# Optimization experiments

Measured on AMD Instinct MI355X. Metric: run time of the kernel, lower is better.

## Reference

```python
import jax, jax.numpy as jnp
import numpy as np

N_NODES = 100000
N_EDGES = 1600000
IN_DIM = 75
H_COMP = 64
H_BOND = 16
DEPTH = 3


def setup_inputs() -> dict:
    key = jax.random.key(0)
    ks = jax.random.split(key, 8)
    x = jax.random.normal(ks[0], (N_NODES, IN_DIM), dtype=jnp.float32)
    edge_index = jax.random.randint(ks[1], (2, N_EDGES), 0, N_NODES, dtype=jnp.int64)
    edge_attr = jax.random.normal(ks[2], (N_EDGES, H_BOND), dtype=jnp.float32)
    proj_w = jax.random.normal(ks[3], (IN_DIM, H_COMP), dtype=jnp.float32) * (1.0 / np.sqrt(IN_DIM))
    proj_b = jnp.zeros((H_COMP,), dtype=jnp.float32)
    u2_w = jax.random.normal(ks[4], (DEPTH, H_COMP + H_BOND, H_COMP), dtype=jnp.float32) * (1.0 / np.sqrt(H_COMP + H_BOND))
    u2_b = jnp.zeros((DEPTH, H_COMP), dtype=jnp.float32)
    u1_w = jax.random.normal(ks[5], (DEPTH, 2 * H_COMP, H_COMP), dtype=jnp.float32) * (1.0 / np.sqrt(2 * H_COMP))
    u1_b = jnp.zeros((DEPTH, H_COMP), dtype=jnp.float32)
    return {"x": x, "edge_index": edge_index, "edge_attr": edge_attr,
            "proj_w": proj_w, "proj_b": proj_b,
            "u2_w": u2_w, "u2_b": u2_b, "u1_w": u1_w, "u1_b": u1_b}


def reference(x, edge_index, edge_attr, proj_w, proj_b, u2_w, u2_b, u1_w, u1_b):
    # PyG default flow source_to_target: messages gathered from edge_index[0],
    # scatter-added at edge_index[1].
    src, dst = edge_index[0], edge_index[1]
    n = x.shape[0]
    # input projection: [N, in_dim] -> [N, H]
    h = x @ proj_w + proj_b
    for l in range(u2_w.shape[0]):
        # message: concat(x_j, edge_attr) -> Linear -> LeakyReLU(0.1)   [E, H+B] -> [E, H]
        z = jnp.concatenate([h[src], edge_attr], axis=-1)
        m = jax.nn.leaky_relu(z @ u2_w[l] + u2_b[l], negative_slope=0.1)
        # aggregate: scatter-add over destination nodes  [E, H] -> [N, H]
        agg = jax.ops.segment_sum(m, dst, num_segments=n)
        # update: concat(x, agg) -> Linear  [N, 2H] -> [N, H]
        h = jnp.concatenate([h, agg], axis=-1) @ u1_w[l] + u1_b[l]
    return h
```

## Files before the change

kernel.cpp:

```cpp
#include <hip/hip_runtime.h>

typedef __attribute__((ext_vector_type(8))) short frag_ab;
typedef __attribute__((ext_vector_type(4))) float frag_cd;

__device__ __forceinline__ short f2bf(float f) {
  union { float f; unsigned u; } v; v.f = f;
  unsigned r = v.u + 0x7fffu + ((v.u >> 16) & 1u);
  return (short)(r >> 16);
}
__device__ __forceinline__ float bf2f(short s) {
  union { unsigned u; float f; } v; v.u = ((unsigned)(unsigned short)s) << 16;
  return v.f;
}

__device__ __forceinline__ void wconv_body(
    const float* __restrict__ W, short* __restrict__ out,
    int Keff, int S, int nmat, int tid)
{
  int per = S * 4 * 64;
  if (tid >= nmat * per) return;
  int m = tid / per, r = tid % per;
  int s = r / 256, ct = (r >> 6) & 3, ln = r & 63;
  const float* Wm = W + (size_t)m * Keff * 64;
  __align__(16) short tmp[8];
  for (int j = 0; j < 8; ++j) {
    int k = s * 32 + (ln >> 4) * 8 + j;
    int n = ct * 16 + (ln & 15);
    tmp[j] = (k < Keff) ? f2bf(Wm[k * 64 + n]) : (short)0;
  }
  *(uint4*)&out[((size_t)m * per + (size_t)(s * 4 + ct) * 64 + ln) * 8] = *(uint4*)tmp;
}

__global__ void wconv_all(const float* __restrict__ pw,
                          const float* __restrict__ u2w,
                          const float* __restrict__ u1w,
                          short* projt, short* u2t, short* u1t)
{
  int b = blockIdx.x, t = threadIdx.x;
  if (b < 3)        wconv_body(pw,  projt, 75,  3, 1, b * 256 + t);
  else if (b < 12)  wconv_body(u2w, u2t,   80,  3, 3, (b - 3) * 256 + t);
  else              wconv_body(u1w, u1t,   128, 4, 3, (b - 12) * 256 + t);
}

#define AS1 104
__global__ __launch_bounds__(256, 4) void proj_kernel(
    const float* __restrict__ x, const short* __restrict__ wt,
    const float* __restrict__ bias, short* __restrict__ hbf, int N)
{
  __shared__ __align__(16) short A[128 * AS1];
  int t = threadIdx.x;
  int nb = blockIdx.x * 128;
  int ln = t & 63;
  frag_ab bf[12];
  for (int s = 0; s < 3; ++s)
    for (int ct = 0; ct < 4; ++ct)
      bf[s * 4 + ct] = *(const frag_ab*)&wt[((size_t)(s * 4 + ct) * 64 + ln) * 8];
  for (int i = 0; i < 48; ++i) {
    int q = i * 256 + t; int el = q / 96; int c = q - el * 96;
    int rg = nb + el;
    float v = (c < 75 && rg < N) ? x[rg * 75 + c] : 0.f;
    A[el * AS1 + c] = f2bf(v);
  }
  __syncthreads();
  int wv = t >> 6;
  int lrow = ln & 15, lk = ln >> 4;
  frag_cd acc[2][4];
  for (int rt = 0; rt < 2; ++rt) for (int ct = 0; ct < 4; ++ct) {
    frag_cd z = {0.f, 0.f, 0.f, 0.f}; acc[rt][ct] = z;
  }
  for (int s = 0; s < 3; ++s) {
    frag_ab a0 = *(const frag_ab*)&A[(wv*32 + lrow) * AS1 + s*32 + lk*8];
    frag_ab a1 = *(const frag_ab*)&A[(wv*32 + 16 + lrow) * AS1 + s*32 + lk*8];
    for (int ct = 0; ct < 4; ++ct) {
      acc[0][ct] = __builtin_amdgcn_mfma_f32_16x16x32_bf16(a0, bf[s*4+ct], acc[0][ct], 0, 0, 0);
      acc[1][ct] = __builtin_amdgcn_mfma_f32_16x16x32_bf16(a1, bf[s*4+ct], acc[1][ct], 0, 0, 0);
    }
  }
  float bv[4];
  for (int ct = 0; ct < 4; ++ct) bv[ct] = bias[ct*16 + lrow];
  for (int rt = 0; rt < 2; ++rt)
    for (int ct = 0; ct < 4; ++ct)
      for (int r = 0; r < 4; ++r) {
        int row = wv*32 + rt*16 + lk*4 + r;
        int rg = nb + row;
        if (rg < N) hbf[(size_t)rg * 64 + ct*16 + lrow] = f2bf(acc[rt][ct][r] + bv[ct]);
      }
}

__global__ __launch_bounds__(256) void hist_kernel(
    const int* __restrict__ dst, int* __restrict__ counts,
    int* __restrict__ rank, int E)
{
  int i = blockIdx.x * 256 + threadIdx.x;
  if (i < E) rank[i] = atomicAdd(&counts[dst[i]], 1);
}

#define SCAN_TILE 2048
__global__ __launch_bounds__(256) void scan_k1(
    const int* __restrict__ counts, int* __restrict__ offsets,
    int* __restrict__ bsum, int n)
{
  __shared__ int ts[256];
  int t = threadIdx.x;
  int base = blockIdx.x * SCAN_TILE + t * 8;
  int v[8]; int s = 0;
  for (int j = 0; j < 8; ++j) { v[j] = (base + j < n) ? counts[base + j] : 0; s += v[j]; }
  ts[t] = s; __syncthreads();
  for (int off = 1; off < 256; off <<= 1) {
    int x = (t >= off) ? ts[t - off] : 0;
    __syncthreads();
    ts[t] += x;
    __syncthreads();
  }
  if (t == 255) bsum[blockIdx.x] = ts[255];
  int run = (t > 0) ? ts[t - 1] : 0;
  for (int j = 0; j < 8; ++j) { if (base + j < n) offsets[base + j] = run; run += v[j]; }
}

__global__ __launch_bounds__(256) void scan_k3(
    int* __restrict__ offsets, const int* __restrict__ bsum, int n, int nb)
{
  __shared__ int adds;
  int t = threadIdx.x;
  if (t < 64) {
    int v = (t < nb) ? bsum[t] : 0;
    int x = v;
    for (int o = 1; o < 64; o <<= 1) { int y = __shfl_up(x, o); if (t >= o) x += y; }
    int b = blockIdx.x;
    int a = __shfl(x, b - 1);
    if (t == 0) adds = (b == 0) ? 0 : a;
  }
  __syncthreads();
  int add = adds;
  int base = blockIdx.x * SCAN_TILE + t;
  for (int j = 0; j < 8; ++j) { int i = base + j * 256; if (i < n) offsets[i] += add; }
}

__global__ __launch_bounds__(256) void scatter_kernel(
    const int* __restrict__ src, const int* __restrict__ dst,
    const float* __restrict__ attr, const int* __restrict__ offsets,
    const int* __restrict__ rank, uint4* __restrict__ rec, int E)
{
  int e = blockIdx.x * 256 + threadIdx.x;
  if (e < E) {
    int d = dst[e];
    int p = offsets[d] + rank[e];
    const float4* a4 = (const float4*)(attr + (size_t)e * 16);
    float4 v0 = a4[0], v1 = a4[1], v2 = a4[2], v3 = a4[3];
    __align__(16) short tmp[16];
    tmp[0]=f2bf(v0.x); tmp[1]=f2bf(v0.y); tmp[2]=f2bf(v0.z); tmp[3]=f2bf(v0.w);
    tmp[4]=f2bf(v1.x); tmp[5]=f2bf(v1.y); tmp[6]=f2bf(v1.z); tmp[7]=f2bf(v1.w);
    tmp[8]=f2bf(v2.x); tmp[9]=f2bf(v2.y); tmp[10]=f2bf(v2.z); tmp[11]=f2bf(v2.w);
    tmp[12]=f2bf(v3.x); tmp[13]=f2bf(v3.y); tmp[14]=f2bf(v3.z); tmp[15]=f2bf(v3.w);
    uint4* rp = rec + (size_t)p * 4;
    uint4 q0; q0.x = (unsigned)src[e]; q0.y = (unsigned)d; q0.z = 0u; q0.w = 0u;
    uint4 qz = {0u, 0u, 0u, 0u};
    rp[0] = q0;
    rp[1] = *(uint4*)&tmp[0];
    rp[2] = *(uint4*)&tmp[8];
    rp[3] = qz;
  }
}

#define MS 66
__global__ __launch_bounds__(256, 6) void msg_kernel(
    const short* __restrict__ hbf, const uint4* __restrict__ rec,
    const short* __restrict__ wt, const float* __restrict__ bias,
    float* __restrict__ agg, int E)
{
  __shared__ short M2[128 * MS];
  int t = threadIdx.x;
  int eb = blockIdx.x * 128;
  int ln = t & 63;
  int wv = t >> 6;
  int lrow = ln & 15, lk = ln >> 4;
  int lo = wv * 32;

  int g0 = eb + lo + lrow;
  int g1 = g0 + 16;
  int p0 = g0 > E - 1 ? E - 1 : g0;
  int p1 = g1 > E - 1 ? E - 1 : g1;
  int2 sd0 = *(const int2*)(rec + (size_t)p0 * 4);
  int2 sd1 = *(const int2*)(rec + (size_t)p1 * 4);
  int d0 = (g0 < E) ? sd0.y : -1;
  int d1 = (g1 < E) ? sd1.y : -1;

  frag_ab a[3][2];
  a[0][0] = *(const frag_ab*)&hbf[(size_t)sd0.x * 64 + lk*8];
  a[0][1] = *(const frag_ab*)&hbf[(size_t)sd1.x * 64 + lk*8];
  a[1][0] = *(const frag_ab*)&hbf[(size_t)sd0.x * 64 + 32 + lk*8];
  a[1][1] = *(const frag_ab*)&hbf[(size_t)sd1.x * 64 + 32 + lk*8];
  frag_ab z8 = {0,0,0,0,0,0,0,0};
  a[2][0] = (lk < 2) ? *(const frag_ab*)((const short*)(rec + (size_t)p0 * 4) + 8 + lk*8) : z8;
  a[2][1] = (lk < 2) ? *(const frag_ab*)((const short*)(rec + (size_t)p1 * 4) + 8 + lk*8) : z8;

  frag_cd acc[2][4];
  for (int rt = 0; rt < 2; ++rt) for (int ct = 0; ct < 4; ++ct) {
    frag_cd z = {0.f, 0.f, 0.f, 0.f}; acc[rt][ct] = z;
  }
  for (int s = 0; s < 3; ++s)
    for (int ct = 0; ct < 4; ++ct) {
      frag_ab b = *(const frag_ab*)&wt[((size_t)(s * 4 + ct) * 64 + ln) * 8];
      acc[0][ct] = __builtin_amdgcn_mfma_f32_16x16x32_bf16(a[s][0], b, acc[0][ct], 0, 0, 0);
      acc[1][ct] = __builtin_amdgcn_mfma_f32_16x16x32_bf16(a[s][1], b, acc[1][ct], 0, 0, 0);
    }
  float bv[4];
  for (int ct = 0; ct < 4; ++ct) bv[ct] = bias[ct*16 + lrow];

  for (int rt = 0; rt < 2; ++rt)
    for (int ct = 0; ct < 4; ++ct)
      for (int r = 0; r < 4; ++r) {
        int row = lo + rt*16 + lk*4 + r;
        float m = acc[rt][ct][r] + bv[ct];
        m = m > 0.f ? m : 0.1f * m;
        M2[row * MS + ct*16 + lrow] = f2bf(m);
      }
  __asm__ __volatile__("s_waitcnt lgkmcnt(0)" ::: "memory");

  int dl = (ln < 16) ? d0 : d1;
  int dnext = __shfl_down(dl, 1);
  bool end = (ln < 32) && ((ln == 31) || (dl != dnext));
  unsigned em = (unsigned)__ballot(end);
  unsigned cm = em & ~(em & (0u - em)) & 0x7fffffffu;

  float s = 0.f;
#pragma unroll
  for (int i = 0; i < 32; ++i) {
    s += bf2f(M2[(lo + i) * MS + ln]);
    if ((em >> i) & 1u) {
      int di = (i < 16) ? __shfl(d0, i) : __shfl(d1, i - 16);
      if (di >= 0) {
        float* dest = &agg[(size_t)di * 64 + ln];
        if ((cm >> i) & 1u) *dest = s;
        else unsafeAtomicAdd(dest, s);
      }
      s = 0.f;
    }
  }
}

__global__ __launch_bounds__(256, 4) void upd_kernel(
    const short* __restrict__ hbf, float* __restrict__ agg,
    const short* __restrict__ wt, const float* __restrict__ bias,
    float* __restrict__ hout, short* __restrict__ hbfo, int N, int last)
{
  int t = threadIdx.x;
  int nb = blockIdx.x * 64;
  int ln = t & 63;
  int wv = t >> 6;
  int lrow = ln & 15, lk = ln >> 4;
  int r0 = nb + wv*16 + lrow;

  frag_ab z8 = {0,0,0,0,0,0,0,0};
  frag_ab a[4];
  a[0] = (r0 < N) ? *(const frag_ab*)&hbf[(size_t)r0 * 64 + lk*8]      : z8;
  a[1] = (r0 < N) ? *(const frag_ab*)&hbf[(size_t)r0 * 64 + 32 + lk*8] : z8;
  for (int si = 0; si < 2; ++si) {
    int cb = si * 32 + lk * 8;
    frag_ab af = z8;
    if (r0 < N) {
      float* ap = &agg[(size_t)r0 * 64 + cb];
      float4 v0 = *(const float4*)ap;
      float4 v1 = *(const float4*)(ap + 4);
      af[0]=f2bf(v0.x); af[1]=f2bf(v0.y); af[2]=f2bf(v0.z); af[3]=f2bf(v0.w);
      af[4]=f2bf(v1.x); af[5]=f2bf(v1.y); af[6]=f2bf(v1.z); af[7]=f2bf(v1.w);
      if (!last) {
        float4 z = make_float4(0.f, 0.f, 0.f, 0.f);
        *(float4*)ap = z; *(float4*)(ap + 4) = z;
      }
    }
    a[2 + si] = af;
  }

  frag_cd acc[4];
  for (int ct = 0; ct < 4; ++ct) {
    frag_cd z = {0.f, 0.f, 0.f, 0.f}; acc[ct] = z;
  }
  for (int s = 0; s < 4; ++s)
    for (int ct = 0; ct < 4; ++ct) {
      frag_ab b = *(const frag_ab*)&wt[((size_t)(s * 4 + ct) * 64 + ln) * 8];
      acc[ct] = __builtin_amdgcn_mfma_f32_16x16x32_bf16(a[s], b, acc[ct], 0, 0, 0);
    }
  float bv[4];
  for (int ct = 0; ct < 4; ++ct) bv[ct] = bias[ct*16 + lrow];
  for (int ct = 0; ct < 4; ++ct)
    for (int r = 0; r < 4; ++r) {
      int rg = nb + wv*16 + lk*4 + r;
      if (rg < N) {
        float v = acc[ct][r] + bv[ct];
        if (last) hout[(size_t)rg * 64 + ct*16 + lrow] = v;
        hbfo[(size_t)rg * 64 + ct*16 + lrow] = f2bf(v);
      }
    }
}

extern "C" void kernel_launch(void* const* d_in, const int* in_sizes, int n_in,
                              void* d_out, int out_size, void* d_ws, size_t ws_size,
                              hipStream_t stream) {
  const float* x    = (const float*)d_in[0];
  const int*   ei   = (const int*)d_in[1];
  const float* attr = (const float*)d_in[2];
  const float* pw   = (const float*)d_in[3];
  const float* pb   = (const float*)d_in[4];
  const float* u2w  = (const float*)d_in[5];
  const float* u2b  = (const float*)d_in[6];
  const float* u1w  = (const float*)d_in[7];
  const float* u1b  = (const float*)d_in[8];

  const int N = in_sizes[0] / 75;
  const int E = in_sizes[1] / 2;
  const int* src = ei;
  const int* dst = ei + E;

  float* hout = (float*)d_out;
  char*  ws   = (char*)d_ws;
  size_t nh   = (size_t)N * 64;
  size_t off  = 0;
  short* hbf   = (short*)(ws + off); off += nh * 2;
  float* agg   = (float*)(ws + off); off += nh * 4;
  uint4* rec   = (uint4*)(ws + off); off += (size_t)E * 64;
  short* projt = (short*)(ws + off); off += 3 * 4 * 64 * 8 * 2;
  short* u2t   = (short*)(ws + off); off += (size_t)3 * 3 * 4 * 64 * 8 * 2;
  short* u1t   = (short*)(ws + off); off += (size_t)3 * 4 * 4 * 64 * 8 * 2;
  int* counts  = (int*)agg;
  int* offsets = counts + N;
  int* bsum    = offsets + N;
  int* rank    = bsum + 64;

  const int NB = (N + 127) / 128;
  const int NB2 = (N + 63) / 64;
  const int EB = (E + 127) / 128;
  const int GE = (E + 255) / 256;
  const int NS = (N + SCAN_TILE - 1) / SCAN_TILE;

  wconv_all<<<24, 256, 0, stream>>>(pw, u2w, u1w, projt, u2t, u1t);
  proj_kernel<<<NB, 256, 0, stream>>>(x, projt, pb, hbf, N);
  hipMemsetAsync(counts, 0, (size_t)N * 4, stream);
  hist_kernel<<<GE, 256, 0, stream>>>(dst, counts, rank, E);
  scan_k1<<<NS, 256, 0, stream>>>(counts, offsets, bsum, N);
  scan_k3<<<NS, 256, 0, stream>>>(offsets, bsum, N, NS);
  scatter_kernel<<<GE, 256, 0, stream>>>(src, dst, attr, offsets, rank, rec, E);

  hipMemsetAsync(agg, 0, nh * 4, stream);
  for (int l = 0; l < 3; ++l) {
    msg_kernel<<<EB, 256, 0, stream>>>(hbf, rec,
                                       u2t + (size_t)l * 6144, u2b + l * 64,
                                       agg, E);
    upd_kernel<<<NB2, 256, 0, stream>>>(hbf, agg,
                                        u1t + (size_t)l * 8192, u1b + l * 64,
                                        hout, hbf, N, l == 2);
  }
}
```

Before: 647.1 us.

## Split sorted edge records into compact index array and unsorted bf16 attribute array

Edge attributes are now converted to bf16 in the histogram pass and stored in original edge order, while the sorted record shrinks from 64 to 16 bytes (src, dst, original edge id). The scatter pass writes only the small record instead of a 64-byte record with padding. The message kernel now fetches the attribute row indirectly through the stored edge id, which turns a sequential read into a random gather on each of the three layers.

```diff
diff --git a/kernel.cpp b/kernel.cpp
--- a/kernel.cpp
+++ b/kernel.cpp
@@ -88,11 +88,24 @@
 }
 
 __global__ __launch_bounds__(256) void hist_kernel(
-    const int* __restrict__ dst, int* __restrict__ counts,
-    int* __restrict__ rank, int E)
+    const int* __restrict__ dst, const float* __restrict__ attr,
+    int* __restrict__ counts, int* __restrict__ rank,
+    uint4* __restrict__ abf, int E)
 {
   int i = blockIdx.x * 256 + threadIdx.x;
-  if (i < E) rank[i] = atomicAdd(&counts[dst[i]], 1);
+  if (i < E) {
+    rank[i] = atomicAdd(&counts[dst[i]], 1);
+    const float4* a4 = (const float4*)(attr + (size_t)i * 16);
+    float4 v0 = a4[0], v1 = a4[1], v2 = a4[2], v3 = a4[3];
+    __align__(16) short tmp[16];
+    tmp[0]=f2bf(v0.x); tmp[1]=f2bf(v0.y); tmp[2]=f2bf(v0.z); tmp[3]=f2bf(v0.w);
+    tmp[4]=f2bf(v1.x); tmp[5]=f2bf(v1.y); tmp[6]=f2bf(v1.z); tmp[7]=f2bf(v1.w);
+    tmp[8]=f2bf(v2.x); tmp[9]=f2bf(v2.y); tmp[10]=f2bf(v2.z); tmp[11]=f2bf(v2.w);
+    tmp[12]=f2bf(v3.x); tmp[13]=f2bf(v3.y); tmp[14]=f2bf(v3.z); tmp[15]=f2bf(v3.w);
+    uint4* rp = abf + (size_t)i * 2;
+    rp[0] = *(uint4*)&tmp[0];
+    rp[1] = *(uint4*)&tmp[8];
+  }
 }
 
 #define SCAN_TILE 2048
@@ -138,33 +151,21 @@
 
 __global__ __launch_bounds__(256) void scatter_kernel(
     const int* __restrict__ src, const int* __restrict__ dst,
-    const float* __restrict__ attr, const int* __restrict__ offsets,
-    const int* __restrict__ rank, uint4* __restrict__ rec, int E)
+    const int* __restrict__ offsets, const int* __restrict__ rank,
+    int4* __restrict__ rec4, int E)
 {
   int e = blockIdx.x * 256 + threadIdx.x;
   if (e < E) {
     int d = dst[e];
     int p = offsets[d] + rank[e];
-    const float4* a4 = (const float4*)(attr + (size_t)e * 16);
-    float4 v0 = a4[0], v1 = a4[1], v2 = a4[2], v3 = a4[3];
-    __align__(16) short tmp[16];
-    tmp[0]=f2bf(v0.x); tmp[1]=f2bf(v0.y); tmp[2]=f2bf(v0.z); tmp[3]=f2bf(v0.w);
-    tmp[4]=f2bf(v1.x); tmp[5]=f2bf(v1.y); tmp[6]=f2bf(v1.z); tmp[7]=f2bf(v1.w);
-    tmp[8]=f2bf(v2.x); tmp[9]=f2bf(v2.y); tmp[10]=f2bf(v2.z); tmp[11]=f2bf(v2.w);
-    tmp[12]=f2bf(v3.x); tmp[13]=f2bf(v3.y); tmp[14]=f2bf(v3.z); tmp[15]=f2bf(v3.w);
-    uint4* rp = rec + (size_t)p * 4;
-    uint4 q0; q0.x = (unsigned)src[e]; q0.y = (unsigned)d; q0.z = 0u; q0.w = 0u;
-    uint4 qz = {0u, 0u, 0u, 0u};
-    rp[0] = q0;
-    rp[1] = *(uint4*)&tmp[0];
-    rp[2] = *(uint4*)&tmp[8];
-    rp[3] = qz;
+    rec4[p] = make_int4(src[e], d, e, 0);
   }
 }
 
 #define MS 66
 __global__ __launch_bounds__(256, 6) void msg_kernel(
-    const short* __restrict__ hbf, const uint4* __restrict__ rec,
+    const short* __restrict__ hbf, const int4* __restrict__ rec4,
+    const uint4* __restrict__ abf,
     const short* __restrict__ wt, const float* __restrict__ bias,
     float* __restrict__ agg, int E)
 {
@@ -180,8 +181,8 @@
   int g1 = g0 + 16;
   int p0 = g0 > E - 1 ? E - 1 : g0;
   int p1 = g1 > E - 1 ? E - 1 : g1;
-  int2 sd0 = *(const int2*)(rec + (size_t)p0 * 4);
-  int2 sd1 = *(const int2*)(rec + (size_t)p1 * 4);
+  int4 sd0 = rec4[p0];
+  int4 sd1 = rec4[p1];
   int d0 = (g0 < E) ? sd0.y : -1;
   int d1 = (g1 < E) ? sd1.y : -1;
 
@@ -191,8 +192,8 @@
   a[1][0] = *(const frag_ab*)&hbf[(size_t)sd0.x * 64 + 32 + lk*8];
   a[1][1] = *(const frag_ab*)&hbf[(size_t)sd1.x * 64 + 32 + lk*8];
   frag_ab z8 = {0,0,0,0,0,0,0,0};
-  a[2][0] = (lk < 2) ? *(const frag_ab*)((const short*)(rec + (size_t)p0 * 4) + 8 + lk*8) : z8;
-  a[2][1] = (lk < 2) ? *(const frag_ab*)((const short*)(rec + (size_t)p1 * 4) + 8 + lk*8) : z8;
+  a[2][0] = (lk < 2) ? *(const frag_ab*)((const short*)abf + (size_t)sd0.z * 16 + lk*8) : z8;
+  a[2][1] = (lk < 2) ? *(const frag_ab*)((const short*)abf + (size_t)sd1.z * 16 + lk*8) : z8;
 
   frag_cd acc[2][4];
   for (int rt = 0; rt < 2; ++rt) for (int ct = 0; ct < 4; ++ct) {
@@ -318,7 +319,8 @@
   size_t off  = 0;
   short* hbf   = (short*)(ws + off); off += nh * 2;
   float* agg   = (float*)(ws + off); off += nh * 4;
-  uint4* rec   = (uint4*)(ws + off); off += (size_t)E * 64;
+  int4*  rec4  = (int4*)(ws + off);  off += (size_t)E * 16;
+  uint4* abf   = (uint4*)(ws + off); off += (size_t)E * 32;
   short* projt = (short*)(ws + off); off += 3 * 4 * 64 * 8 * 2;
   short* u2t   = (short*)(ws + off); off += (size_t)3 * 3 * 4 * 64 * 8 * 2;
   short* u1t   = (short*)(ws + off); off += (size_t)3 * 4 * 4 * 64 * 8 * 2;
@@ -336,14 +338,14 @@
   wconv_all<<<24, 256, 0, stream>>>(pw, u2w, u1w, projt, u2t, u1t);
   proj_kernel<<<NB, 256, 0, stream>>>(x, projt, pb, hbf, N);
   hipMemsetAsync(counts, 0, (size_t)N * 4, stream);
-  hist_kernel<<<GE, 256, 0, stream>>>(dst, counts, rank, E);
+  hist_kernel<<<GE, 256, 0, stream>>>(dst, attr, counts, rank, abf, E);
   scan_k1<<<NS, 256, 0, stream>>>(counts, offsets, bsum, N);
   scan_k3<<<NS, 256, 0, stream>>>(offsets, bsum, N, NS);
-  scatter_kernel<<<GE, 256, 0, stream>>>(src, dst, attr, offsets, rank, rec, E);
+  scatter_kernel<<<GE, 256, 0, stream>>>(src, dst, offsets, rank, rec4, E);
 
   hipMemsetAsync(agg, 0, nh * 4, stream);
   for (int l = 0; l < 3; ++l) {
-    msg_kernel<<<EB, 256, 0, stream>>>(hbf, rec,
+    msg_kernel<<<EB, 256, 0, stream>>>(hbf, rec4, abf,
                                        u2t + (size_t)l * 6144, u2b + l * 64,
                                        agg, E);
     upd_kernel<<<NB2, 256, 0, stream>>>(hbf, agg,
```

Result: slower. 678.5 us (+4.9%).
